# Performance work log

Measured on AMD Instinct MI355X. Metric: run time of the kernel, lower is better.

Reference implementation:

```python
import jax, jax.numpy as jnp
import numpy as np


def setup_inputs() -> dict:
    key = jax.random.key(0)
    k1, k2 = jax.random.split(key)
    N, K, E = 65536, 8, 64  # tokens, top_k, num_experts
    top_scores = jax.random.normal(k1, (N, K), dtype=jnp.float32)
    selected_experts_indices = jax.random.randint(k2, (N, K), 0, E, dtype=jnp.int32)
    return {
        "top_scores": top_scores,
        "selected_experts_indices": selected_experts_indices,
        "num_experts": E,
        "top_k": K,
    }


def reference(top_scores, selected_experts_indices, num_experts, top_k):
    # Flatten (token, slot) assignments: total = N * top_k
    expert_flat = selected_experts_indices.reshape(-1)

    # Histogram: number of assignments per expert (float32, matching torch impl)
    num_tokens_per_expert = jax.ops.segment_sum(
        jnp.ones_like(expert_flat, dtype=jnp.float32),
        expert_flat,
        num_segments=num_experts,
    )

    # Stable sort by expert id == counting sort: for each output slot, which
    # flattened assignment index lands there. Identical to the torch
    # scatter/cumsum counting-sort since both are stable.
    token_indices_experts_sorted = jnp.argsort(expert_flat, stable=True)

    # Gather routing scores into expert-sorted order
    top_scores_experts_sorted = top_scores.reshape(-1)[token_indices_experts_sorted]

    # Map flattened assignment index back to token index
    token_indices_experts_sorted = token_indices_experts_sorted // top_k

    return (top_scores_experts_sorted, token_indices_experts_sorted, num_tokens_per_expert)
```

## Files before the change

kernel.cpp:

```cpp
#include <hip/hip_runtime.h>

#define TOTAL   524288
#define NEXP    64
#define TOPK    8
#define GSIZE   256
#define BLOCK   1024
#define NWAVE   16
#define CHUNK   (TOTAL / GSIZE)
#define ROWSPW  (GSIZE / NWAVE)

__device__ __forceinline__ unsigned long long expert_mask(
        const unsigned long long bb[6], int x) {
    unsigned long long m = ~0ULL;
#pragma unroll
    for (int bit = 0; bit < 6; bit++)
        m &= ((x >> bit) & 1) ? bb[bit] : ~bb[bit];
    return m;
}

__global__ __launch_bounds__(BLOCK) void hist_kernel(const int* __restrict__ idx,
                                                     int* __restrict__ counts) {
    __shared__ int hist[NWAVE][NEXP];
    const int tid = threadIdx.x, lane = tid & 63, wave = tid >> 6;

    const int2 e2 = ((const int2*)idx)[blockIdx.x * (CHUNK / 2) + tid];

    unsigned long long bb0[6], bb1[6];
#pragma unroll
    for (int bit = 0; bit < 6; bit++) {
        bb0[bit] = __ballot((e2.x >> bit) & 1);
        bb1[bit] = __ballot((e2.y >> bit) & 1);
    }
    hist[wave][lane] = __popcll(expert_mask(bb0, lane)) +
                       __popcll(expert_mask(bb1, lane));
    __syncthreads();
    if (tid < NEXP) {
        int s = 0;
#pragma unroll
        for (int w = 0; w < NWAVE; w++) s += hist[w][tid];
        counts[blockIdx.x * NEXP + tid] = s;
    }
}

__global__ __launch_bounds__(BLOCK) void scatter_kernel(
        const float* __restrict__ scores,
        const int*   __restrict__ idx,
        const int*   __restrict__ counts,
        float*       __restrict__ out_scores,
        float*       __restrict__ out_tok,
        float*       __restrict__ out_cnt) {
    __shared__ int   wtot[NWAVE][NEXP];
    __shared__ int   part_pre[NWAVE][NEXP];
    __shared__ int   part_tot[NWAVE][NEXP];
    __shared__ int   exscan_pre[NEXP];
    __shared__ float sc_s[CHUNK];
    __shared__ float tk_s[CHUNK];
    __shared__ int   gp_s[CHUNK];

    const int tid = threadIdx.x, lane = tid & 63, wave = tid >> 6, b = blockIdx.x;
    const unsigned long long lt  = (1ULL << lane) - 1ULL;
    const unsigned long long own = 1ULL << lane;

    const int2   e2 = ((const int2*)idx)[b * (CHUNK / 2) + tid];
    const float2 s2 = ((const float2*)scores)[b * (CHUNK / 2) + tid];

    int pre = 0, tot = 0;
    {
        const int r0 = wave * ROWSPW;
#pragma unroll
        for (int q = 0; q < ROWSPW; q++) {
            const int bb = r0 + q;
            const int c  = counts[bb * NEXP + lane];
            tot += c;
            pre += (bb < b) ? c : 0;
        }
    }
    part_pre[wave][lane] = pre;
    part_tot[wave][lane] = tot;

    const int e0 = e2.x, e1 = e2.y;
    unsigned long long bb0[6], bb1[6];
#pragma unroll
    for (int bit = 0; bit < 6; bit++) {
        bb0[bit] = __ballot((e0 >> bit) & 1);
        bb1[bit] = __ballot((e1 >> bit) & 1);
    }
    const unsigned long long M0 = expert_mask(bb0, lane);
    const unsigned long long M1 = expert_mask(bb1, lane);
    wtot[wave][lane] = __popcll(M0) + __popcll(M1);
    __syncthreads();

    int t_pre_w = 0, t_blk = 0;
#pragma unroll
    for (int w = 0; w < NWAVE; w++) {
        const int c = wtot[w][lane];
        t_pre_w += (w < wave) ? c : 0;
        t_blk   += c;
    }
    int linc = t_blk;
#pragma unroll
    for (int d = 1; d < 64; d <<= 1) {
        const int v = __shfl_up(linc, d, 64);
        if (lane >= d) linc += v;
    }
    const int base_local = (linc - t_blk) + t_pre_w;

    if (wave == 0) {
        int p = 0, t = 0;
#pragma unroll
        for (int w = 0; w < NWAVE; w++) {
            p += part_pre[w][lane];
            t += part_tot[w][lane];
        }
        if (b == 0) out_cnt[lane] = (float)t;
        int inc = t;
#pragma unroll
        for (int d = 1; d < 64; d <<= 1) {
            const int v = __shfl_up(inc, d, 64);
            if (lane >= d) inc += v;
        }
        exscan_pre[lane] = (inc - t) + p;
    }
    __syncthreads();

    const int base_glob = exscan_pre[lane] + t_pre_w;

    const unsigned long long own0 = __shfl(M0, e0, 64);
    const unsigned long long own1 = __shfl(M1, e1, 64);
    const unsigned long long c01  = __shfl(M1, e0, 64);
    const unsigned long long c10  = __shfl(M0, e1, 64);
    const int bl0 = __shfl(base_local, e0, 64);
    const int bl1 = __shfl(base_local, e1, 64);
    const int bg0 = __shfl(base_glob, e0, 64);
    const int bg1 = __shfl(base_glob, e1, 64);

    const int rank0 = __popcll(own0 & lt) + __popcll(c01 & lt);
    const int rank1 = __popcll(c10 & (lt | own)) + __popcll(own1 & lt);

    const int f0 = b * CHUNK + 2 * tid;
    const int l0 = bl0 + rank0, l1 = bl1 + rank1;
    const int g0 = bg0 + rank0, g1 = bg1 + rank1;

    sc_s[l0] = s2.x;             sc_s[l1] = s2.y;
    tk_s[l0] = (float)(f0 >> 3); tk_s[l1] = (float)((f0 + 1) >> 3);
    gp_s[l0] = g0;               gp_s[l1] = g1;
    __syncthreads();

#pragma unroll
    for (int r = 0; r < 2; r++) {
        const int i = tid + r * BLOCK;
        const int p = gp_s[i];
        out_scores[p] = sc_s[i];
        out_tok[p]    = tk_s[i];
    }
}

extern "C" void kernel_launch(void* const* d_in, const int* in_sizes, int n_in,
                              void* d_out, int out_size, void* d_ws, size_t ws_size,
                              hipStream_t stream) {
    const float* top_scores = (const float*)d_in[0];
    const int*   sel_idx    = (const int*)d_in[1];
    float*       out        = (float*)d_out;
    int*         counts     = (int*)d_ws;

    float* out_scores = out;
    float* out_tok    = out + TOTAL;
    float* out_cnt    = out + 2 * TOTAL;

    hist_kernel<<<GSIZE, BLOCK, 0, stream>>>(sel_idx, counts);
    scatter_kernel<<<GSIZE, BLOCK, 0, stream>>>(top_scores, sel_idx, counts,
                                                out_scores, out_tok, out_cnt);
}
```

Measured before the change: 66.63 us.

## Fuse histogram and scatter kernels with a flag-based grid barrier

```diff
diff --git a/kernel.cpp b/kernel.cpp
--- a/kernel.cpp
+++ b/kernel.cpp
@@ -9,43 +9,21 @@
 #define CHUNK   (TOTAL / GSIZE)
 #define ROWSPW  (GSIZE / NWAVE)
 
-__device__ __forceinline__ unsigned long long expert_mask(
-        const unsigned long long bb[6], int x) {
-    unsigned long long m = ~0ULL;
+typedef unsigned long long ull;
+
+__device__ __forceinline__ ull expert_mask(const ull bb[6], int x) {
+    ull m = ~0ULL;
 #pragma unroll
     for (int bit = 0; bit < 6; bit++)
         m &= ((x >> bit) & 1) ? bb[bit] : ~bb[bit];
     return m;
 }
 
-__global__ __launch_bounds__(BLOCK) void hist_kernel(const int* __restrict__ idx,
-                                                     int* __restrict__ counts) {
-    __shared__ int hist[NWAVE][NEXP];
-    const int tid = threadIdx.x, lane = tid & 63, wave = tid >> 6;
-
-    const int2 e2 = ((const int2*)idx)[blockIdx.x * (CHUNK / 2) + tid];
-
-    unsigned long long bb0[6], bb1[6];
-#pragma unroll
-    for (int bit = 0; bit < 6; bit++) {
-        bb0[bit] = __ballot((e2.x >> bit) & 1);
-        bb1[bit] = __ballot((e2.y >> bit) & 1);
-    }
-    hist[wave][lane] = __popcll(expert_mask(bb0, lane)) +
-                       __popcll(expert_mask(bb1, lane));
-    __syncthreads();
-    if (tid < NEXP) {
-        int s = 0;
-#pragma unroll
-        for (int w = 0; w < NWAVE; w++) s += hist[w][tid];
-        counts[blockIdx.x * NEXP + tid] = s;
-    }
-}
-
-__global__ __launch_bounds__(BLOCK) void scatter_kernel(
+__global__ __launch_bounds__(BLOCK) void fused_kernel(
         const float* __restrict__ scores,
         const int*   __restrict__ idx,
-        const int*   __restrict__ counts,
+        int*         __restrict__ counts,
+        int*         __restrict__ flags,
         float*       __restrict__ out_scores,
         float*       __restrict__ out_tok,
         float*       __restrict__ out_cnt) {
@@ -58,37 +36,34 @@
     __shared__ int   gp_s[CHUNK];
 
     const int tid = threadIdx.x, lane = tid & 63, wave = tid >> 6, b = blockIdx.x;
-    const unsigned long long lt  = (1ULL << lane) - 1ULL;
-    const unsigned long long own = 1ULL << lane;
+    const ull lt  = (1ULL << lane) - 1ULL;
+    const ull own = 1ULL << lane;
 
     const int2   e2 = ((const int2*)idx)[b * (CHUNK / 2) + tid];
     const float2 s2 = ((const float2*)scores)[b * (CHUNK / 2) + tid];
 
-    int pre = 0, tot = 0;
-    {
-        const int r0 = wave * ROWSPW;
-#pragma unroll
-        for (int q = 0; q < ROWSPW; q++) {
-            const int bb = r0 + q;
-            const int c  = counts[bb * NEXP + lane];
-            tot += c;
-            pre += (bb < b) ? c : 0;
-        }
-    }
-    part_pre[wave][lane] = pre;
-    part_tot[wave][lane] = tot;
-
     const int e0 = e2.x, e1 = e2.y;
-    unsigned long long bb0[6], bb1[6];
+    ull bb0[6], bb1[6];
 #pragma unroll
     for (int bit = 0; bit < 6; bit++) {
         bb0[bit] = __ballot((e0 >> bit) & 1);
         bb1[bit] = __ballot((e1 >> bit) & 1);
     }
-    const unsigned long long M0 = expert_mask(bb0, lane);
-    const unsigned long long M1 = expert_mask(bb1, lane);
+    const ull M0 = expert_mask(bb0, lane);
+    const ull M1 = expert_mask(bb1, lane);
     wtot[wave][lane] = __popcll(M0) + __popcll(M1);
     __syncthreads();
+
+    if (wave == 0) {
+        int t = 0;
+#pragma unroll
+        for (int w = 0; w < NWAVE; w++) t += wtot[w][lane];
+        __hip_atomic_store(&counts[b * NEXP + lane], t,
+                           __ATOMIC_RELAXED, __HIP_MEMORY_SCOPE_AGENT);
+        if (lane == 0)
+            __hip_atomic_store(&flags[b], 1,
+                               __ATOMIC_RELEASE, __HIP_MEMORY_SCOPE_AGENT);
+    }
 
     int t_pre_w = 0, t_blk = 0;
 #pragma unroll
@@ -104,6 +79,50 @@
         if (lane >= d) linc += v;
     }
     const int base_local = (linc - t_blk) + t_pre_w;
+
+    const ull own0 = __shfl(M0, e0, 64);
+    const ull own1 = __shfl(M1, e1, 64);
+    const ull c01  = __shfl(M1, e0, 64);
+    const ull c10  = __shfl(M0, e1, 64);
+    const int bl0  = __shfl(base_local, e0, 64);
+    const int bl1  = __shfl(base_local, e1, 64);
+
+    const int rank0 = __popcll(own0 & lt) + __popcll(c01 & lt);
+    const int rank1 = __popcll(c10 & (lt | own)) + __popcll(own1 & lt);
+
+    const int f0 = b * CHUNK + 2 * tid;
+    const int l0 = bl0 + rank0, l1 = bl1 + rank1;
+
+    sc_s[l0] = s2.x;             sc_s[l1] = s2.y;
+    tk_s[l0] = (float)(f0 >> 3); tk_s[l1] = (float)((f0 + 1) >> 3);
+
+    if (wave == 0) {
+        int got;
+        do {
+            got = 0;
+#pragma unroll
+            for (int j = 0; j < 4; j++)
+                got += __hip_atomic_load(&flags[lane * 4 + j],
+                                         __ATOMIC_ACQUIRE, __HIP_MEMORY_SCOPE_AGENT);
+        } while (!__all(got == 4));
+    }
+    __syncthreads();
+
+    int pre = 0, tot = 0;
+    {
+        const int r0 = wave * ROWSPW;
+#pragma unroll
+        for (int q = 0; q < ROWSPW; q++) {
+            const int bb = r0 + q;
+            const int c  = __hip_atomic_load(&counts[bb * NEXP + lane],
+                                             __ATOMIC_RELAXED, __HIP_MEMORY_SCOPE_AGENT);
+            tot += c;
+            pre += (bb < b) ? c : 0;
+        }
+    }
+    part_pre[wave][lane] = pre;
+    part_tot[wave][lane] = tot;
+    __syncthreads();
 
     if (wave == 0) {
         int p = 0, t = 0;
@@ -124,26 +143,10 @@
     __syncthreads();
 
     const int base_glob = exscan_pre[lane] + t_pre_w;
-
-    const unsigned long long own0 = __shfl(M0, e0, 64);
-    const unsigned long long own1 = __shfl(M1, e1, 64);
-    const unsigned long long c01  = __shfl(M1, e0, 64);
-    const unsigned long long c10  = __shfl(M0, e1, 64);
-    const int bl0 = __shfl(base_local, e0, 64);
-    const int bl1 = __shfl(base_local, e1, 64);
     const int bg0 = __shfl(base_glob, e0, 64);
     const int bg1 = __shfl(base_glob, e1, 64);
-
-    const int rank0 = __popcll(own0 & lt) + __popcll(c01 & lt);
-    const int rank1 = __popcll(c10 & (lt | own)) + __popcll(own1 & lt);
-
-    const int f0 = b * CHUNK + 2 * tid;
-    const int l0 = bl0 + rank0, l1 = bl1 + rank1;
-    const int g0 = bg0 + rank0, g1 = bg1 + rank1;
-
-    sc_s[l0] = s2.x;             sc_s[l1] = s2.y;
-    tk_s[l0] = (float)(f0 >> 3); tk_s[l1] = (float)((f0 + 1) >> 3);
-    gp_s[l0] = g0;               gp_s[l1] = g1;
+    gp_s[l0] = bg0 + rank0;
+    gp_s[l1] = bg1 + rank1;
     __syncthreads();
 
 #pragma unroll
@@ -161,13 +164,14 @@
     const float* top_scores = (const float*)d_in[0];
     const int*   sel_idx    = (const int*)d_in[1];
     float*       out        = (float*)d_out;
-    int*         counts     = (int*)d_ws;
+    int*         flags      = (int*)d_ws;
+    int*         counts     = (int*)d_ws + 256;
 
     float* out_scores = out;
     float* out_tok    = out + TOTAL;
     float* out_cnt    = out + 2 * TOTAL;
 
-    hist_kernel<<<GSIZE, BLOCK, 0, stream>>>(sel_idx, counts);
-    scatter_kernel<<<GSIZE, BLOCK, 0, stream>>>(top_scores, sel_idx, counts,
-                                                out_scores, out_tok, out_cnt);
+    hipMemsetAsync(flags, 0, GSIZE * sizeof(int), stream);
+    fused_kernel<<<GSIZE, BLOCK, 0, stream>>>(top_scores, sel_idx, counts, flags,
+                                              out_scores, out_tok, out_cnt);
 }
```

Result: slower. 82.25 us (+23.4%).
